# Optimization experiments

Hardware: AMD Instinct MI355X
Metric: run time of the kernel (lower is better)

The kernel has to match this reference:

```python
import jax, jax.numpy as jnp
import numpy as np

TEN_PI = 10.0 * np.pi

def _normalize(x):
    # Normalize each column to [-1, 1]
    x_min = jnp.min(x, axis=0, keepdims=True)
    x_max = jnp.max(x, axis=0, keepdims=True)
    x_range = x_max - x_min
    x_range = jnp.where(x_range == 0, jnp.ones_like(x_range), x_range)
    return 2.0 * (x - x_min) / x_range - 1.0

def _basis_features(xn):
    # 9 elementwise basis functions, stacked on last axis -> [N, d, 9]
    feats = [
        xn,
        jnp.clip(xn ** 2, -100.0, 100.0),
        jnp.clip(xn ** 3, -100.0, 100.0),
        jnp.exp(jnp.clip(xn, -10.0, 10.0)),
        jnp.log(jnp.abs(xn) + 1.0),
        jnp.sqrt(jnp.abs(xn)),
        jnp.tanh(xn),
        jnp.sin(jnp.clip(xn, -TEN_PI, TEN_PI)),
        jnp.abs(xn),
    ]
    return jnp.stack(feats, axis=-1)

def setup_inputs() -> dict:
    key = jax.random.key(0)
    k1, k2 = jax.random.split(key)
    N, d, K = 1000000, 16, 9
    x = jax.random.normal(k1, (N, d), dtype=jnp.float32)
    weights = jax.random.normal(k2, (K,), dtype=jnp.float32) * 0.1
    bias = jnp.zeros((1,), dtype=jnp.float32)
    return {"x": x, "weights": weights, "bias": bias}

def reference(x, weights, bias):
    xn = _normalize(x)                 # [N, d]
    features = _basis_features(xn)     # [N, d, 9]
    out = jnp.einsum('ndk,k->nd', features, weights)[..., None] + bias  # [N, d, 1]
    return out
```

## Files before the change

kernel.cpp:

```cpp
#include <hip/hip_runtime.h>
#include <stdint.h>

#define NCOL 16
typedef float v4f __attribute__((ext_vector_type(4)));

__device__ __forceinline__ uint32_t fkey(float f) {
    uint32_t u = __float_as_uint(f);
    return (u & 0x80000000u) ? ~u : (u | 0x80000000u);
}
__device__ __forceinline__ float fkey_dec(uint32_t k) {
    uint32_t u = (k & 0x80000000u) ? (k ^ 0x80000000u) : ~k;
    return __uint_as_float(u);
}

__global__ void __launch_bounds__(256) colreduce(const v4f* __restrict__ x,
                                                 uint32_t* __restrict__ mm, int n4) {
    int tid = blockIdx.x * blockDim.x + threadIdx.x;
    int stride = gridDim.x * blockDim.x;
    float mn0 = INFINITY, mn1 = INFINITY, mn2 = INFINITY, mn3 = INFINITY;
    float mx0 = -INFINITY, mx1 = -INFINITY, mx2 = -INFINITY, mx3 = -INFINITY;
    for (int i = tid; i < n4; i += stride) {
        v4f v = x[i];
        mn0 = fminf(mn0, v.x); mx0 = fmaxf(mx0, v.x);
        mn1 = fminf(mn1, v.y); mx1 = fmaxf(mx1, v.y);
        mn2 = fminf(mn2, v.z); mx2 = fmaxf(mx2, v.z);
        mn3 = fminf(mn3, v.w); mx3 = fmaxf(mx3, v.w);
    }
    #pragma unroll
    for (int off = 4; off < 64; off <<= 1) {
        mn0 = fminf(mn0, __shfl_xor(mn0, off)); mx0 = fmaxf(mx0, __shfl_xor(mx0, off));
        mn1 = fminf(mn1, __shfl_xor(mn1, off)); mx1 = fmaxf(mx1, __shfl_xor(mx1, off));
        mn2 = fminf(mn2, __shfl_xor(mn2, off)); mx2 = fmaxf(mx2, __shfl_xor(mx2, off));
        mn3 = fminf(mn3, __shfl_xor(mn3, off)); mx3 = fmaxf(mx3, __shfl_xor(mx3, off));
    }
    __shared__ float smn[4][NCOL], smx[4][NCOL];
    int wave = threadIdx.x >> 6;
    int lane = threadIdx.x & 63;
    if (lane < 4) {
        int g = lane * 4;
        smn[wave][g + 0] = mn0; smx[wave][g + 0] = mx0;
        smn[wave][g + 1] = mn1; smx[wave][g + 1] = mx1;
        smn[wave][g + 2] = mn2; smx[wave][g + 2] = mx2;
        smn[wave][g + 3] = mn3; smx[wave][g + 3] = mx3;
    }
    __syncthreads();
    if (threadIdx.x < NCOL) {
        int c = threadIdx.x;
        float m = fminf(fminf(smn[0][c], smn[1][c]), fminf(smn[2][c], smn[3][c]));
        float M = fmaxf(fmaxf(smx[0][c], smx[1][c]), fmaxf(smx[2][c], smx[3][c]));
        atomicMin(&mm[c], fkey(m));
        atomicMin(&mm[NCOL + c], fkey(-M));
    }
}

__device__ __forceinline__ float eval_basis(float xn, const float* w, float b) {
    float ax = fabsf(xn);
    float x2 = xn * xn;
    float x3 = x2 * xn;
    float e  = __expf(xn);
    float e2 = e * e;
    float t  = 1.0f - 2.0f * __frcp_rn(e2 + 1.0f);
    float l  = __logf(ax + 1.0f);
    float sq = __fsqrt_rn(ax);
    float sn = __sinf(xn);
    float r = b;
    r = fmaf(w[0], xn, r);
    r = fmaf(w[1], x2, r);
    r = fmaf(w[2], x3, r);
    r = fmaf(w[3], e,  r);
    r = fmaf(w[4], l,  r);
    r = fmaf(w[5], sq, r);
    r = fmaf(w[6], t,  r);
    r = fmaf(w[7], sn, r);
    r = fmaf(w[8], ax, r);
    return r;
}

__global__ void __launch_bounds__(256) feature_kernel(const v4f* __restrict__ x,
                                                      v4f* __restrict__ out,
                                                      const uint32_t* __restrict__ mm,
                                                      const float* __restrict__ wts,
                                                      const float* __restrict__ bias,
                                                      int n4) {
    __shared__ float s_scale[NCOL], s_off[NCOL], s_w[9];
    if (threadIdx.x < NCOL) {
        float mn = fkey_dec(mm[threadIdx.x]);
        float mx = -fkey_dec(mm[NCOL + threadIdx.x]);
        float r = mx - mn;
        if (r == 0.0f) r = 1.0f;
        s_scale[threadIdx.x] = 2.0f / r;
        s_off[threadIdx.x]   = -2.0f * mn / r - 1.0f;
    }
    if (threadIdx.x < 9) s_w[threadIdx.x] = wts[threadIdx.x];
    __syncthreads();

    int tid = blockIdx.x * blockDim.x + threadIdx.x;
    int stride = gridDim.x * blockDim.x;
    int g = (tid & 3) * 4;
    float sc0 = s_scale[g + 0], of0 = s_off[g + 0];
    float sc1 = s_scale[g + 1], of1 = s_off[g + 1];
    float sc2 = s_scale[g + 2], of2 = s_off[g + 2];
    float sc3 = s_scale[g + 3], of3 = s_off[g + 3];
    float w[9];
    #pragma unroll
    for (int k = 0; k < 9; ++k) w[k] = s_w[k];
    float b = bias[0];

    for (int i = tid; i < n4; i += stride) {
        v4f v = x[i];
        v4f o;
        o.x = eval_basis(fmaf(v.x, sc0, of0), w, b);
        o.y = eval_basis(fmaf(v.y, sc1, of1), w, b);
        o.z = eval_basis(fmaf(v.z, sc2, of2), w, b);
        o.w = eval_basis(fmaf(v.w, sc3, of3), w, b);
        __builtin_nontemporal_store(o, &out[i]);
    }
}

extern "C" void kernel_launch(void* const* d_in, const int* in_sizes, int n_in,
                              void* d_out, int out_size, void* d_ws, size_t ws_size,
                              hipStream_t stream) {
    const float* x    = (const float*)d_in[0];
    const float* wts  = (const float*)d_in[1];
    const float* bias = (const float*)d_in[2];
    float* out = (float*)d_out;
    uint32_t* mm = (uint32_t*)d_ws;

    int n  = in_sizes[0];
    int n4 = n / 4;

    hipMemsetAsync(mm, 0xFF, 2 * NCOL * sizeof(uint32_t), stream);

    colreduce<<<2048, 256, 0, stream>>>((const v4f*)x, mm, n4);
    feature_kernel<<<4096, 256, 0, stream>>>((const v4f*)x, (v4f*)out, mm,
                                             wts, bias, n4);
}
```

Measured before the change: 149.5 us.

## Fuse column min/max reduction and feature evaluation into one persistent kernel

Merges the reduction and feature kernels into a single persistent launch of 1024 blocks that uses software grid barriers. Per-block min/max results go to slots and are combined in a two-level tree instead of through global atomicMin on ordered keys. This removes one kernel launch and the atomic contention, but adds the cost of spin-wait barriers. Correctness depends on all 1024 blocks being resident at the same time, which the launch bounds are meant to guarantee.

```diff
diff --git a/kernel.cpp b/kernel.cpp
--- a/kernel.cpp
+++ b/kernel.cpp
@@ -2,55 +2,20 @@
 #include <stdint.h>
 
 #define NCOL 16
+#define GRID 1024
+#define NRED 32
 typedef float v4f __attribute__((ext_vector_type(4)));
 
-__device__ __forceinline__ uint32_t fkey(float f) {
-    uint32_t u = __float_as_uint(f);
-    return (u & 0x80000000u) ? ~u : (u | 0x80000000u);
-}
-__device__ __forceinline__ float fkey_dec(uint32_t k) {
-    uint32_t u = (k & 0x80000000u) ? (k ^ 0x80000000u) : ~k;
-    return __uint_as_float(u);
-}
-
-__global__ void __launch_bounds__(256) colreduce(const v4f* __restrict__ x,
-                                                 uint32_t* __restrict__ mm, int n4) {
-    int tid = blockIdx.x * blockDim.x + threadIdx.x;
-    int stride = gridDim.x * blockDim.x;
-    float mn0 = INFINITY, mn1 = INFINITY, mn2 = INFINITY, mn3 = INFINITY;
-    float mx0 = -INFINITY, mx1 = -INFINITY, mx2 = -INFINITY, mx3 = -INFINITY;
-    for (int i = tid; i < n4; i += stride) {
-        v4f v = x[i];
-        mn0 = fminf(mn0, v.x); mx0 = fmaxf(mx0, v.x);
-        mn1 = fminf(mn1, v.y); mx1 = fmaxf(mx1, v.y);
-        mn2 = fminf(mn2, v.z); mx2 = fmaxf(mx2, v.z);
-        mn3 = fminf(mn3, v.w); mx3 = fmaxf(mx3, v.w);
-    }
-    #pragma unroll
-    for (int off = 4; off < 64; off <<= 1) {
-        mn0 = fminf(mn0, __shfl_xor(mn0, off)); mx0 = fmaxf(mx0, __shfl_xor(mx0, off));
-        mn1 = fminf(mn1, __shfl_xor(mn1, off)); mx1 = fmaxf(mx1, __shfl_xor(mx1, off));
-        mn2 = fminf(mn2, __shfl_xor(mn2, off)); mx2 = fmaxf(mx2, __shfl_xor(mx2, off));
-        mn3 = fminf(mn3, __shfl_xor(mn3, off)); mx3 = fmaxf(mx3, __shfl_xor(mx3, off));
-    }
-    __shared__ float smn[4][NCOL], smx[4][NCOL];
-    int wave = threadIdx.x >> 6;
-    int lane = threadIdx.x & 63;
-    if (lane < 4) {
-        int g = lane * 4;
-        smn[wave][g + 0] = mn0; smx[wave][g + 0] = mx0;
-        smn[wave][g + 1] = mn1; smx[wave][g + 1] = mx1;
-        smn[wave][g + 2] = mn2; smx[wave][g + 2] = mx2;
-        smn[wave][g + 3] = mn3; smx[wave][g + 3] = mx3;
+__device__ __forceinline__ void arrive_and_wait(uint32_t* ctr) {
+    __syncthreads();
+    if (threadIdx.x == 0) {
+        asm volatile("s_waitcnt vmcnt(0)" ::: "memory");
+        __hip_atomic_fetch_add(ctr, 1u, __ATOMIC_RELAXED, __HIP_MEMORY_SCOPE_AGENT);
+        while (__hip_atomic_load(ctr, __ATOMIC_RELAXED, __HIP_MEMORY_SCOPE_AGENT) < GRID)
+            __builtin_amdgcn_s_sleep(2);
+        asm volatile("" ::: "memory");
     }
     __syncthreads();
-    if (threadIdx.x < NCOL) {
-        int c = threadIdx.x;
-        float m = fminf(fminf(smn[0][c], smn[1][c]), fminf(smn[2][c], smn[3][c]));
-        float M = fmaxf(fmaxf(smx[0][c], smx[1][c]), fmaxf(smx[2][c], smx[3][c]));
-        atomicMin(&mm[c], fkey(m));
-        atomicMin(&mm[NCOL + c], fkey(-M));
-    }
 }
 
 __device__ __forceinline__ float eval_basis(float xn, const float* w, float b) {
@@ -76,26 +41,114 @@
     return r;
 }
 
-__global__ void __launch_bounds__(256) feature_kernel(const v4f* __restrict__ x,
-                                                      v4f* __restrict__ out,
-                                                      const uint32_t* __restrict__ mm,
-                                                      const float* __restrict__ wts,
-                                                      const float* __restrict__ bias,
-                                                      int n4) {
+__global__ void __launch_bounds__(256, 4) fused(const v4f* __restrict__ x,
+                                                v4f* __restrict__ out,
+                                                uint32_t* __restrict__ ctrs,
+                                                float* __restrict__ slots1,
+                                                float* __restrict__ slots2,
+                                                const float* __restrict__ wts,
+                                                const float* __restrict__ bias,
+                                                int n4) {
+    __shared__ float smn[4][NCOL], smx[4][NCOL];
+    __shared__ float s_red[8][32];
     __shared__ float s_scale[NCOL], s_off[NCOL], s_w[9];
+
+    if (threadIdx.x < 9) s_w[threadIdx.x] = wts[threadIdx.x];
+
+    const int tid = blockIdx.x * 256 + threadIdx.x;
+    const int stride = GRID * 256;
+
+    float mn0 = INFINITY, mn1 = INFINITY, mn2 = INFINITY, mn3 = INFINITY;
+    float mx0 = -INFINITY, mx1 = -INFINITY, mx2 = -INFINITY, mx3 = -INFINITY;
+    for (int i = tid; i < n4; i += stride) {
+        v4f v = x[i];
+        mn0 = fminf(mn0, v.x); mx0 = fmaxf(mx0, v.x);
+        mn1 = fminf(mn1, v.y); mx1 = fmaxf(mx1, v.y);
+        mn2 = fminf(mn2, v.z); mx2 = fmaxf(mx2, v.z);
+        mn3 = fminf(mn3, v.w); mx3 = fmaxf(mx3, v.w);
+    }
+    #pragma unroll
+    for (int off = 4; off < 64; off <<= 1) {
+        mn0 = fminf(mn0, __shfl_xor(mn0, off)); mx0 = fmaxf(mx0, __shfl_xor(mx0, off));
+        mn1 = fminf(mn1, __shfl_xor(mn1, off)); mx1 = fmaxf(mx1, __shfl_xor(mx1, off));
+        mn2 = fminf(mn2, __shfl_xor(mn2, off)); mx2 = fmaxf(mx2, __shfl_xor(mx2, off));
+        mn3 = fminf(mn3, __shfl_xor(mn3, off)); mx3 = fmaxf(mx3, __shfl_xor(mx3, off));
+    }
+    int wave = threadIdx.x >> 6;
+    int lane = threadIdx.x & 63;
+    if (lane < 4) {
+        int g = lane * 4;
+        smn[wave][g + 0] = mn0; smx[wave][g + 0] = mx0;
+        smn[wave][g + 1] = mn1; smx[wave][g + 1] = mx1;
+        smn[wave][g + 2] = mn2; smx[wave][g + 2] = mx2;
+        smn[wave][g + 3] = mn3; smx[wave][g + 3] = mx3;
+    }
+    __syncthreads();
     if (threadIdx.x < NCOL) {
-        float mn = fkey_dec(mm[threadIdx.x]);
-        float mx = -fkey_dec(mm[NCOL + threadIdx.x]);
-        float r = mx - mn;
-        if (r == 0.0f) r = 1.0f;
-        s_scale[threadIdx.x] = 2.0f / r;
-        s_off[threadIdx.x]   = -2.0f * mn / r - 1.0f;
+        int c = threadIdx.x;
+        float m = fminf(fminf(smn[0][c], smn[1][c]), fminf(smn[2][c], smn[3][c]));
+        float M = fmaxf(fmaxf(smx[0][c], smx[1][c]), fmaxf(smx[2][c], smx[3][c]));
+        __hip_atomic_store(&slots1[(size_t)blockIdx.x * 32 + c],        m,
+                           __ATOMIC_RELAXED, __HIP_MEMORY_SCOPE_AGENT);
+        __hip_atomic_store(&slots1[(size_t)blockIdx.x * 32 + NCOL + c], M,
+                           __ATOMIC_RELAXED, __HIP_MEMORY_SCOPE_AGENT);
     }
-    if (threadIdx.x < 9) s_w[threadIdx.x] = wts[threadIdx.x];
-    __syncthreads();
+    arrive_and_wait(&ctrs[0]);
 
-    int tid = blockIdx.x * blockDim.x + threadIdx.x;
-    int stride = gridDim.x * blockDim.x;
+    if (blockIdx.x < NRED) {
+        int j  = threadIdx.x & 31;
+        int r0 = threadIdx.x >> 5;
+        bool isMin = j < NCOL;
+        float acc = isMin ? INFINITY : -INFINITY;
+        #pragma unroll
+        for (int r = r0; r < GRID / NRED; r += 8) {
+            float v = __hip_atomic_load(
+                &slots1[((size_t)blockIdx.x * (GRID / NRED) + r) * 32 + j],
+                __ATOMIC_RELAXED, __HIP_MEMORY_SCOPE_AGENT);
+            acc = isMin ? fminf(acc, v) : fmaxf(acc, v);
+        }
+        s_red[r0][j] = acc;
+        __syncthreads();
+        if (threadIdx.x < 32) {
+            float a = s_red[0][j];
+            #pragma unroll
+            for (int g2 = 1; g2 < 8; ++g2)
+                a = isMin ? fminf(a, s_red[g2][j]) : fmaxf(a, s_red[g2][j]);
+            __hip_atomic_store(&slots2[(size_t)blockIdx.x * 32 + j], a,
+                               __ATOMIC_RELAXED, __HIP_MEMORY_SCOPE_AGENT);
+        }
+    }
+    arrive_and_wait(&ctrs[1]);
+
+    {
+        int j  = threadIdx.x & 31;
+        int r0 = threadIdx.x >> 5;
+        bool isMin = j < NCOL;
+        float acc = isMin ? INFINITY : -INFINITY;
+        #pragma unroll
+        for (int r = r0; r < NRED; r += 8) {
+            float v = __hip_atomic_load(&slots2[(size_t)r * 32 + j],
+                                        __ATOMIC_RELAXED, __HIP_MEMORY_SCOPE_AGENT);
+            acc = isMin ? fminf(acc, v) : fmaxf(acc, v);
+        }
+        s_red[r0][j] = acc;
+        __syncthreads();
+        if (threadIdx.x < NCOL) {
+            int c = threadIdx.x;
+            float mn = INFINITY, mx = -INFINITY;
+            #pragma unroll
+            for (int g2 = 0; g2 < 8; ++g2) {
+                mn = fminf(mn, s_red[g2][c]);
+                mx = fmaxf(mx, s_red[g2][NCOL + c]);
+            }
+            float rr = mx - mn;
+            if (rr == 0.0f) rr = 1.0f;
+            s_scale[c] = 2.0f / rr;
+            s_off[c]   = -2.0f * mn / rr - 1.0f;
+        }
+        __syncthreads();
+    }
+
     int g = (tid & 3) * 4;
     float sc0 = s_scale[g + 0], of0 = s_off[g + 0];
     float sc1 = s_scale[g + 1], of1 = s_off[g + 1];
@@ -120,18 +173,19 @@
 extern "C" void kernel_launch(void* const* d_in, const int* in_sizes, int n_in,
                               void* d_out, int out_size, void* d_ws, size_t ws_size,
                               hipStream_t stream) {
-    const float* x    = (const float*)d_in[0];
+    const v4f*   x    = (const v4f*)d_in[0];
     const float* wts  = (const float*)d_in[1];
     const float* bias = (const float*)d_in[2];
-    float* out = (float*)d_out;
-    uint32_t* mm = (uint32_t*)d_ws;
+    v4f* out = (v4f*)d_out;
+
+    uint32_t* ctrs   = (uint32_t*)d_ws;
+    float*    slots1 = (float*)d_ws + 64;
+    float*    slots2 = slots1 + (size_t)GRID * 32;
 
     int n  = in_sizes[0];
     int n4 = n / 4;
 
-    hipMemsetAsync(mm, 0xFF, 2 * NCOL * sizeof(uint32_t), stream);
+    hipMemsetAsync(ctrs, 0, 2 * sizeof(uint32_t), stream);
 
-    colreduce<<<2048, 256, 0, stream>>>((const v4f*)x, mm, n4);
-    feature_kernel<<<4096, 256, 0, stream>>>((const v4f*)x, (v4f*)out, mm,
-                                             wts, bias, n4);
+    fused<<<GRID, 256, 0, stream>>>(x, out, ctrs, slots1, slots2, wts, bias, n4);
 }
```

After: 191.2 us. +27.9%, slower.
